# Kernel tuning notes

Hardware: AMD Instinct MI355X
Metric: run time of the kernel (lower is better)

## Reference

```python
import jax, jax.numpy as jnp
import numpy as np

N = 50000
E = 800000
IN_DIM = 128
EMB_DIM = 64
HID = 128
OUT_DIM = 64
VOCAB = 1000
NUM_GRAPHS = 128


def _gat(x, src, dst, W, a_s, a_d, b, n):
    # PyG GATConv, heads=1: h = x @ W (no bias); alpha_e = leaky_relu(a_s.h_src + a_d.h_dst, 0.2)
    h = x @ W                                  # [n, C]
    as_n = h @ a_s                             # [n]
    ad_n = h @ a_d                             # [n]
    logit = jax.nn.leaky_relu(as_n[src] + ad_n[dst], negative_slope=0.2)  # [E']
    # segment softmax over destination node
    m = jax.ops.segment_max(logit, dst, num_segments=n)
    e = jnp.exp(logit - m[dst])
    s = jax.ops.segment_sum(e, dst, num_segments=n)
    coef = e / s[dst]                          # [E']
    out = jax.ops.segment_sum(h[src] * coef[:, None], dst, num_segments=n)
    return out + b


def setup_inputs() -> dict:
    key = jax.random.key(0)
    ks = jax.random.split(key, 20)
    inp = {
        "x": jax.random.normal(ks[0], (N, IN_DIM), dtype=jnp.float32),
        "node_index": jax.random.randint(ks[1], (N,), 0, VOCAB),
        "edge_index": jax.random.randint(ks[2], (2, E), 0, N),
        "batch": jnp.sort(jax.random.randint(ks[3], (N,), 0, NUM_GRAPHS)),
        "emb": jax.random.normal(ks[4], (VOCAB, EMB_DIM), dtype=jnp.float32) * 0.1,
        "W1": jax.random.normal(ks[5], (IN_DIM + EMB_DIM, HID), dtype=jnp.float32) * 0.05,
        "a1s": jax.random.normal(ks[6], (HID,), dtype=jnp.float32) * 0.1,
        "a1d": jax.random.normal(ks[7], (HID,), dtype=jnp.float32) * 0.1,
        "b1": jnp.zeros((HID,), dtype=jnp.float32),
        "W2": jax.random.normal(ks[8], (HID, HID), dtype=jnp.float32) * 0.05,
        "a2s": jax.random.normal(ks[9], (HID,), dtype=jnp.float32) * 0.1,
        "a2d": jax.random.normal(ks[10], (HID,), dtype=jnp.float32) * 0.1,
        "b2": jnp.zeros((HID,), dtype=jnp.float32),
        "W3": jax.random.normal(ks[11], (HID, HID), dtype=jnp.float32) * 0.05,
        "a3s": jax.random.normal(ks[12], (HID,), dtype=jnp.float32) * 0.1,
        "a3d": jax.random.normal(ks[13], (HID,), dtype=jnp.float32) * 0.1,
        "b3": jnp.zeros((HID,), dtype=jnp.float32),
        "fcW": jax.random.normal(ks[14], (HID, OUT_DIM), dtype=jnp.float32) * 0.05,
        "fcb": jnp.zeros((OUT_DIM,), dtype=jnp.float32),
    }
    return inp


def reference(x, node_index, edge_index, batch, emb, W1, a1s, a1d, b1,
              W2, a2s, a2d, b2, W3, a3s, a3d, b3, fcW, fcb):
    n = x.shape[0]
    # embedding lookup + L2 normalize features, then concat
    ev = emb[node_index]                       # [N, EMB_DIM]
    norms = jnp.linalg.norm(x, axis=1, keepdims=True)
    norms = jnp.where(norms == 0, 1e-8, norms)
    h = jnp.concatenate([x / norms, ev], axis=1)  # [N, IN+EMB]
    # add self loops (PyG GATConv default add_self_loops=True)
    loop = jnp.arange(n)
    src = jnp.concatenate([edge_index[0], loop])
    dst = jnp.concatenate([edge_index[1], loop])
    h = jax.nn.gelu(_gat(h, src, dst, W1, a1s, a1d, b1, n))
    h = jax.nn.gelu(_gat(h, src, dst, W2, a2s, a2d, b2, n))
    h = jax.nn.gelu(_gat(h, src, dst, W3, a3s, a3d, b3, n))
    # global_add_pool over graphs
    g = jax.ops.segment_sum(h, batch, num_segments=NUM_GRAPHS)  # [G, HID]
    out = g @ fcW + fcb
    return jax.nn.leaky_relu(out, negative_slope=0.01)
```

## Files before the change

kernel.cpp:

```cpp
#include <hip/hip_runtime.h>

#define N_NODES 50000
#define N_EDGES 800000
#define IN_DIM 128
#define EMB_DIM 64
#define HID 128
#define OUT_DIM 64
#define NUM_GRAPHS 128
#define E_TOT (N_EDGES + N_NODES)
#define K1 (IN_DIM + EMB_DIM)
#define NB 391
#define EPT 16
#define EPB (256 * EPT)

typedef __attribute__((ext_vector_type(8))) short bf16x8;
typedef __attribute__((ext_vector_type(4))) float f32x4;

__device__ __forceinline__ float gelu_f(float x) {
    float x3 = x * x * x;
    return 0.5f * x * (1.0f + tanhf(0.7978845608028654f * (x + 0.044715f * x3)));
}
__device__ __forceinline__ float lrelu02(float x) { return x > 0.f ? x : 0.2f * x; }
__device__ __forceinline__ float rl_f(float v, int j) {
    return __int_as_float(__builtin_amdgcn_readlane(__float_as_int(v), j));
}
__device__ __forceinline__ unsigned short f2bf(float f) {
    unsigned u = __float_as_uint(f);
    unsigned r = (u + 0x7fffu + ((u >> 16) & 1u)) >> 16;
    return (unsigned short)r;
}
__device__ __forceinline__ unsigned pk2bf(float a, float b) {
    return (unsigned)f2bf(a) | ((unsigned)f2bf(b) << 16);
}

__global__ __launch_bounds__(256) void k_prepA(const float* __restrict__ x, const int* __restrict__ nidx,
                                               const float* __restrict__ emb, unsigned* __restrict__ Abu) {
    int lane = threadIdx.x & 63;
    int node = (blockIdx.x * 256 + threadIdx.x) >> 6;
    if (node >= N_NODES) return;
    float2 v = ((const float2*)(x + (size_t)node * IN_DIM))[lane];
    float ss = v.x * v.x + v.y * v.y;
#pragma unroll
    for (int o = 32; o; o >>= 1) ss += __shfl_xor(ss, o);
    float nrm = sqrtf(ss);
    if (nrm == 0.f) nrm = 1e-8f;
    float inv = 1.f / nrm;
    unsigned* row = Abu + (size_t)node * (K1 / 2);
    row[lane] = pk2bf(v.x * inv, v.y * inv);
    int nid = __builtin_amdgcn_readfirstlane(nidx[node]);
    if (lane < 32) {
        float2 e = ((const float2*)(emb + (size_t)nid * EMB_DIM))[lane];
        row[64 + lane] = pk2bf(e.x, e.y);
    }
}

__global__ __launch_bounds__(128) void k_prepW(const float* __restrict__ W, unsigned short* __restrict__ Wt,
                                               int K, int KP) {
    int k = blockIdx.x;
    int c = threadIdx.x;
    Wt[(size_t)c * KP + k] = f2bf(W[(size_t)k * HID + c]);
}

__global__ __launch_bounds__(256) void k_bhist(const int* __restrict__ dst, int* __restrict__ bcnt) {
    __shared__ int h[NB];
    for (int i = threadIdx.x; i < NB; i += 256) h[i] = 0;
    __syncthreads();
    for (int e = blockIdx.x * 256 + threadIdx.x; e < N_EDGES; e += gridDim.x * 256)
        atomicAdd(&h[dst[e] >> 7], 1);
    __syncthreads();
    for (int i = threadIdx.x; i < NB; i += 256)
        if (h[i]) atomicAdd(&bcnt[i], h[i]);
}

__global__ __launch_bounds__(512) void k_bscan(const int* __restrict__ bcnt, int* __restrict__ boff,
                                               int* __restrict__ rowptr) {
    __shared__ int sh[512];
    int t = threadIdx.x;
    int v = (t < NB) ? bcnt[t] : 0;
    sh[t] = v;
    __syncthreads();
    for (int o = 1; o < 512; o <<= 1) {
        int u = (t >= o) ? sh[t - o] : 0;
        __syncthreads();
        sh[t] += u;
        __syncthreads();
    }
    if (t < NB) boff[t] = sh[t] - v;
    if (t == NB - 1) boff[NB] = sh[t];
    if (t == 0) rowptr[N_NODES] = E_TOT;
}

__global__ __launch_bounds__(256) void k_passA(const int* __restrict__ src, const int* __restrict__ dst,
                                               const int* __restrict__ boff, int* __restrict__ bfill,
                                               unsigned* __restrict__ barr) {
    __shared__ int h[NB];
    __shared__ int base[NB];
    for (int i = threadIdx.x; i < NB; i += 256) h[i] = 0;
    __syncthreads();
    int e0 = blockIdx.x * EPB;
    int tag[EPT];
#pragma unroll
    for (int i = 0; i < EPT; i++) {
        int e = e0 + i * 256 + threadIdx.x;
        tag[i] = -1;
        if (e < N_EDGES) {
            int b = dst[e] >> 7;
            int r = atomicAdd(&h[b], 1);
            tag[i] = (b << 12) | r;
        }
    }
    __syncthreads();
    for (int i = threadIdx.x; i < NB; i += 256)
        base[i] = h[i] ? atomicAdd(&bfill[i], h[i]) : 0;
    __syncthreads();
#pragma unroll
    for (int i = 0; i < EPT; i++) {
        if (tag[i] >= 0) {
            int e = e0 + i * 256 + threadIdx.x;
            int b = tag[i] >> 12, r = tag[i] & 0xfff;
            unsigned s = (unsigned)src[e];
            unsigned dl = (unsigned)(dst[e] & 127);
            barr[boff[b] + base[b] + r] = s | (dl << 16);
        }
    }
}

__global__ __launch_bounds__(256) void k_passB(const unsigned* __restrict__ barr, const int* __restrict__ boff,
                                               int* __restrict__ rowptr, int* __restrict__ csr) {
    __shared__ int dcnt[128];
    __shared__ int dsum[128];
    __shared__ int locOff[128];
    int b = blockIdx.x;
    int t = threadIdx.x;
    int n0 = b << 7;
    int cnt = min(128, N_NODES - n0);
    int eb = boff[b], ee = boff[b + 1];
    if (t < 128) dcnt[t] = 0;
    __syncthreads();
    for (int i = eb + t; i < ee; i += 256) atomicAdd(&dcnt[barr[i] >> 16], 1);
    __syncthreads();
    int v = 0;
    if (t < 128) {
        v = (t < cnt) ? dcnt[t] + 1 : 0;
        dsum[t] = v;
    }
    __syncthreads();
    for (int o = 1; o < 128; o <<= 1) {
        int u = (t >= o && t < 128) ? dsum[t - o] : 0;
        __syncthreads();
        if (t < 128) dsum[t] += u;
        __syncthreads();
    }
    int csrBase = eb + n0;
    if (t < 128) {
        locOff[t] = dsum[t] - v;
        dcnt[t] = 0;
    }
    if (t < cnt) {
        int loc = dsum[t] - v;
        rowptr[n0 + t] = csrBase + loc;
        csr[csrBase + loc] = n0 + t;
    }
    __syncthreads();
    for (int i = eb + t; i < ee; i += 256) {
        unsigned vv = barr[i];
        int dl = vv >> 16;
        int s = (int)(vv & 0xffffu);
        int k = atomicAdd(&dcnt[dl], 1);
        csr[csrBase + locOff[dl] + 1 + k] = s;
    }
}

template <int K>
__global__ __launch_bounds__(256) void k_mgemm(const unsigned short* __restrict__ Abf,
                                               const unsigned short* __restrict__ WtP,
                                               const float* __restrict__ a_s, const float* __restrict__ a_d,
                                               unsigned short* __restrict__ Hbf,
                                               float* __restrict__ asn, float* __restrict__ adn) {
    constexpr int KP = K + 8;
    __shared__ __align__(16) unsigned short Wl[128 * KP];
    {
        const uint4* gsrc = (const uint4*)WtP;
        uint4* ldst = (uint4*)Wl;
        const int nchunk = 128 * KP * 2 / 16;
        for (int i = threadIdx.x; i < nchunk; i += 256) ldst[i] = gsrc[i];
    }
    __syncthreads();
    int lane = threadIdx.x & 63;
    int wv = threadIdx.x >> 6;
    int rowbase = blockIdx.x * 64 + wv * 16;
    if (rowbase >= N_NODES) return;
    int l15 = lane & 15, quad = lane >> 4;

    f32x4 acc[8];
#pragma unroll
    for (int t = 0; t < 8; t++) acc[t] = (f32x4){0.f, 0.f, 0.f, 0.f};

    const unsigned short* Abase = Abf + (size_t)(rowbase + l15) * K + quad * 8;
#pragma unroll
    for (int k0 = 0; k0 < K; k0 += 32) {
        bf16x8 af = *(const bf16x8*)(Abase + k0);
#pragma unroll
        for (int t = 0; t < 8; t++) {
            bf16x8 bf = *(const bf16x8*)(&Wl[(t * 16 + l15) * KP + k0 + quad * 8]);
            acc[t] = __builtin_amdgcn_mfma_f32_16x16x32_bf16(af, bf, acc[t], 0, 0, 0);
        }
    }
    float asc[8], adc[8];
#pragma unroll
    for (int t = 0; t < 8; t++) { asc[t] = a_s[t * 16 + l15]; adc[t] = a_d[t * 16 + l15]; }
#pragma unroll
    for (int r = 0; r < 4; r++) {
        int row = rowbase + quad * 4 + r;
        float ps = 0.f, pd = 0.f;
#pragma unroll
        for (int t = 0; t < 8; t++) {
            float v = acc[t][r];
            Hbf[(size_t)row * HID + t * 16 + l15] = f2bf(v);
            ps = fmaf(v, asc[t], ps);
            pd = fmaf(v, adc[t], pd);
        }
#pragma unroll
        for (int o = 1; o < 16; o <<= 1) {
            ps += __shfl_xor(ps, o);
            pd += __shfl_xor(pd, o);
        }
        if (l15 == 0) { asn[row] = ps; adn[row] = pd; }
    }
}

template <bool OUT32>
__global__ __launch_bounds__(256) void k_aggr(const int* __restrict__ rowptr, const int* __restrict__ csr,
                                              const float* __restrict__ asn, const float* __restrict__ adn,
                                              const unsigned short* __restrict__ hbf,
                                              const float* __restrict__ bias, void* __restrict__ outp) {
    __shared__ float sh_e[4][64];
    __shared__ int sh_s[4][64];
    int lane = threadIdx.x & 63;
    int w = threadIdx.x >> 6;
    int node = blockIdx.x * 4 + w;
    if (node >= N_NODES) return;
    int st = rowptr[node], en = rowptr[node + 1];
    int deg = en - st;
    float ad = adn[node];
    const unsigned* hu = (const unsigned*)hbf;
    float2 acc = make_float2(0.f, 0.f);

    if (deg <= 64) {
        int s = 0;
        float l = -1e30f;
        if (lane < deg) {
            s = csr[st + lane];
            l = lrelu02(asn[s] + ad);
        }
        float m = l;
#pragma unroll
        for (int o = 32; o; o >>= 1) m = fmaxf(m, __shfl_xor(m, o));
        float e = (lane < deg) ? __expf(l - m) : 0.f;
        float ssum = e;
#pragma unroll
        for (int o = 32; o; o >>= 1) ssum += __shfl_xor(ssum, o);
        float coef = e / ssum;
        int j = 0;
        for (; j + 4 <= deg; j += 4) {
            int s0 = __builtin_amdgcn_readlane(s, j);
            int s1 = __builtin_amdgcn_readlane(s, j + 1);
            int s2 = __builtin_amdgcn_readlane(s, j + 2);
            int s3 = __builtin_amdgcn_readlane(s, j + 3);
            float c0 = rl_f(coef, j), c1 = rl_f(coef, j + 1);
            float c2 = rl_f(coef, j + 2), c3 = rl_f(coef, j + 3);
            unsigned v0 = hu[(size_t)s0 * 64 + lane];
            unsigned v1 = hu[(size_t)s1 * 64 + lane];
            unsigned v2 = hu[(size_t)s2 * 64 + lane];
            unsigned v3 = hu[(size_t)s3 * 64 + lane];
            acc.x = fmaf(c0, __int_as_float(v0 << 16), acc.x);
            acc.y = fmaf(c0, __int_as_float(v0 & 0xffff0000u), acc.y);
            acc.x = fmaf(c1, __int_as_float(v1 << 16), acc.x);
            acc.y = fmaf(c1, __int_as_float(v1 & 0xffff0000u), acc.y);
            acc.x = fmaf(c2, __int_as_float(v2 << 16), acc.x);
            acc.y = fmaf(c2, __int_as_float(v2 & 0xffff0000u), acc.y);
            acc.x = fmaf(c3, __int_as_float(v3 << 16), acc.x);
            acc.y = fmaf(c3, __int_as_float(v3 & 0xffff0000u), acc.y);
        }
        for (; j < deg; j++) {
            int s0 = __builtin_amdgcn_readlane(s, j);
            float c0 = rl_f(coef, j);
            unsigned v0 = hu[(size_t)s0 * 64 + lane];
            acc.x = fmaf(c0, __int_as_float(v0 << 16), acc.x);
            acc.y = fmaf(c0, __int_as_float(v0 & 0xffff0000u), acc.y);
        }
    } else {
        float m = -1e30f;
        for (int i = st + lane; i < en; i += 64) {
            float l = lrelu02(asn[csr[i]] + ad);
            m = fmaxf(m, l);
        }
#pragma unroll
        for (int o = 32; o; o >>= 1) m = fmaxf(m, __shfl_xor(m, o));
        float ssum = 0.f;
        for (int i = st + lane; i < en; i += 64) {
            float l = lrelu02(asn[csr[i]] + ad);
            ssum += __expf(l - m);
        }
#pragma unroll
        for (int o = 32; o; o >>= 1) ssum += __shfl_xor(ssum, o);
        float inv = 1.f / ssum;
        for (int base = st; base < en; base += 64) {
            int cnt = min(64, en - base);
            if (lane < cnt) {
                int s = csr[base + lane];
                float l = lrelu02(asn[s] + ad);
                sh_e[w][lane] = __expf(l - m) * inv;
                sh_s[w][lane] = s;
            }
            for (int j = 0; j < cnt; j++) {
                float c = sh_e[w][j];
                int s = sh_s[w][j];
                unsigned v0 = hu[(size_t)s * 64 + lane];
                acc.x = fmaf(c, __int_as_float(v0 << 16), acc.x);
                acc.y = fmaf(c, __int_as_float(v0 & 0xffff0000u), acc.y);
            }
        }
    }
    float2 b = ((const float2*)bias)[lane];
    float rx = gelu_f(acc.x + b.x);
    float ry = gelu_f(acc.y + b.y);
    if constexpr (OUT32) {
        ((float2*)outp)[(size_t)node * 64 + lane] = make_float2(rx, ry);
    } else {
        ((unsigned*)outp)[(size_t)node * 64 + lane] = pk2bf(rx, ry);
    }
}

__global__ __launch_bounds__(128) void k_pool(const float* __restrict__ h, const int* __restrict__ batch,
                                              float* __restrict__ g) {
    int c = threadIdx.x;
    int n0 = blockIdx.x * 128;
    if (n0 >= N_NODES) return;
    int n1 = min(n0 + 128, N_NODES);
    int cur = batch[n0];
    float acc = 0.f;
    for (int n = n0; n < n1; n++) {
        int b = batch[n];
        if (b != cur) {
            atomicAdd(&g[cur * HID + c], acc);
            acc = 0.f;
            cur = b;
        }
        acc += h[(size_t)n * HID + c];
    }
    atomicAdd(&g[cur * HID + c], acc);
}

__global__ __launch_bounds__(256) void k_fc(const float* __restrict__ g, const float* __restrict__ fcW,
                                            const float* __restrict__ fcb, float* __restrict__ out) {
    int tid = blockIdx.x * 256 + threadIdx.x;
    if (tid >= NUM_GRAPHS * OUT_DIM) return;
    int gr = tid >> 6;
    int c = tid & 63;
    float acc = fcb[c];
    const float* grow = g + gr * HID;
#pragma unroll 4
    for (int k = 0; k < HID; k++) acc = fmaf(grow[k], fcW[k * OUT_DIM + c], acc);
    out[tid] = acc > 0.f ? acc : 0.01f * acc;
}

extern "C" void kernel_launch(void* const* d_in, const int* in_sizes, int n_in,
                              void* d_out, int out_size, void* d_ws, size_t ws_size,
                              hipStream_t stream) {
    const float* x    = (const float*)d_in[0];
    const int* nidx   = (const int*)d_in[1];
    const int* ei     = (const int*)d_in[2];
    const int* batch  = (const int*)d_in[3];
    const float* emb  = (const float*)d_in[4];
    const float* W1   = (const float*)d_in[5];
    const float* a1s  = (const float*)d_in[6];
    const float* a1d  = (const float*)d_in[7];
    const float* b1   = (const float*)d_in[8];
    const float* W2   = (const float*)d_in[9];
    const float* a2s  = (const float*)d_in[10];
    const float* a2d  = (const float*)d_in[11];
    const float* b2   = (const float*)d_in[12];
    const float* W3   = (const float*)d_in[13];
    const float* a3s  = (const float*)d_in[14];
    const float* a3d  = (const float*)d_in[15];
    const float* b3   = (const float*)d_in[16];
    const float* fcW  = (const float*)d_in[17];
    const float* fcb  = (const float*)d_in[18];
    float* out = (float*)d_out;
    const int* srcA = ei;
    const int* dstA = ei + N_EDGES;

    char* w = (char*)d_ws;
    auto alloc = [&](size_t bytes) -> char* {
        char* p = w;
        w += (bytes + 511) & ~(size_t)511;
        return p;
    };
    char* region0 = alloc((size_t)N_NODES * HID * 4);
    unsigned* Abu = (unsigned*)region0;
    float* h3f    = (float*)region0;
    unsigned short* hLin = (unsigned short*)alloc((size_t)N_NODES * HID * 2);
    unsigned short* hAct = (unsigned short*)alloc((size_t)N_NODES * HID * 2);
    float* asn   = (float*)alloc((size_t)N_NODES * 4);
    float* adn   = (float*)alloc((size_t)N_NODES * 4);
    int* rowptr  = (int*)alloc((size_t)(N_NODES + 1) * 4);
    int* bcnt    = (int*)alloc((size_t)NB * 4);
    int* boff    = (int*)alloc((size_t)(NB + 1) * 4);
    int* bfill   = (int*)alloc((size_t)NB * 4);
    unsigned* barr = (unsigned*)alloc((size_t)N_EDGES * 4);
    int* csr     = (int*)alloc((size_t)E_TOT * 4);
    float* g     = (float*)alloc((size_t)NUM_GRAPHS * HID * 4);
    unsigned short* Wt1 = (unsigned short*)alloc((size_t)HID * (K1 + 8) * 2);
    unsigned short* Wt2 = (unsigned short*)alloc((size_t)HID * (HID + 8) * 2);
    unsigned short* Wt3 = (unsigned short*)alloc((size_t)HID * (HID + 8) * 2);

    hipMemsetAsync(bcnt, 0, (size_t)NB * 4, stream);
    hipMemsetAsync(bfill, 0, (size_t)NB * 4, stream);
    hipMemsetAsync(g, 0, (size_t)NUM_GRAPHS * HID * 4, stream);

    k_prepW<<<K1, 128, 0, stream>>>(W1, Wt1, K1, K1 + 8);
    k_prepW<<<HID, 128, 0, stream>>>(W2, Wt2, HID, HID + 8);
    k_prepW<<<HID, 128, 0, stream>>>(W3, Wt3, HID, HID + 8);
    k_prepA<<<(N_NODES + 3) / 4, 256, 0, stream>>>(x, nidx, emb, Abu);

    k_bhist<<<512, 256, 0, stream>>>(dstA, bcnt);
    k_bscan<<<1, 512, 0, stream>>>(bcnt, boff, rowptr);
    k_passA<<<(N_EDGES + EPB - 1) / EPB, 256, 0, stream>>>(srcA, dstA, boff, bfill, barr);
    k_passB<<<NB, 256, 0, stream>>>(barr, boff, rowptr, csr);

    int gemmBlocks = (N_NODES + 63) / 64;
    int aggrBlocks = (N_NODES + 3) / 4;

    k_mgemm<K1><<<gemmBlocks, 256, 0, stream>>>((const unsigned short*)Abu, Wt1, a1s, a1d, hLin, asn, adn);
    k_aggr<false><<<aggrBlocks, 256, 0, stream>>>(rowptr, csr, asn, adn, hLin, b1, hAct);
    k_mgemm<HID><<<gemmBlocks, 256, 0, stream>>>(hAct, Wt2, a2s, a2d, hLin, asn, adn);
    k_aggr<false><<<aggrBlocks, 256, 0, stream>>>(rowptr, csr, asn, adn, hLin, b2, hAct);
    k_mgemm<HID><<<gemmBlocks, 256, 0, stream>>>(hAct, Wt3, a3s, a3d, hLin, asn, adn);
    k_aggr<true><<<aggrBlocks, 256, 0, stream>>>(rowptr, csr, asn, adn, hLin, b3, h3f);

    k_pool<<<(N_NODES + 127) / 128, 128, 0, stream>>>(h3f, batch, g);
    k_fc<<<(NUM_GRAPHS * OUT_DIM + 255) / 256, 256, 0, stream>>>(g, fcW, fcb, out);
}
```

Baseline: 372.6 us.

## Merge launches, prefetch GEMM A fragments, unroll gather by 8, fuse pool+fc

Three memsets become one zeroing kernel, and the three weight-transpose launches become one kernel. The GEMM now loads all A fragments before the shared-memory barrier, so global loads overlap the weight staging. The aggregation loop gathers eight neighbours at a time to keep more loads in flight. Pooling and the final FC are fused into one block per graph that binary-searches the sorted batch vector, removing atomics and a launch but leaving only 128 blocks for the pooling pass.

```diff
diff --git a/kernel.cpp b/kernel.cpp
--- a/kernel.cpp
+++ b/kernel.cpp
@@ -33,6 +33,27 @@
     return (unsigned)f2bf(a) | ((unsigned)f2bf(b) << 16);
 }
 
+__global__ __launch_bounds__(256) void k_zero(int* __restrict__ bcnt, int* __restrict__ bfill) {
+    int t = blockIdx.x * 256 + threadIdx.x;
+    if (t < NB) { bcnt[t] = 0; bfill[t] = 0; }
+}
+
+__global__ __launch_bounds__(128) void k_prepW3(const float* __restrict__ W1, unsigned short* __restrict__ Wt1,
+                                                const float* __restrict__ W2, unsigned short* __restrict__ Wt2,
+                                                const float* __restrict__ W3, unsigned short* __restrict__ Wt3) {
+    int b = blockIdx.x;
+    int c = threadIdx.x;
+    if (b < K1) {
+        Wt1[(size_t)c * (K1 + 8) + b] = f2bf(W1[(size_t)b * HID + c]);
+    } else if (b < K1 + HID) {
+        int k = b - K1;
+        Wt2[(size_t)c * (HID + 8) + k] = f2bf(W2[(size_t)k * HID + c]);
+    } else {
+        int k = b - K1 - HID;
+        Wt3[(size_t)c * (HID + 8) + k] = f2bf(W3[(size_t)k * HID + c]);
+    }
+}
+
 __global__ __launch_bounds__(256) void k_prepA(const float* __restrict__ x, const int* __restrict__ nidx,
                                                const float* __restrict__ emb, unsigned* __restrict__ Abu) {
     int lane = threadIdx.x & 63;
@@ -52,13 +73,6 @@
         float2 e = ((const float2*)(emb + (size_t)nid * EMB_DIM))[lane];
         row[64 + lane] = pk2bf(e.x, e.y);
     }
-}
-
-__global__ __launch_bounds__(128) void k_prepW(const float* __restrict__ W, unsigned short* __restrict__ Wt,
-                                               int K, int KP) {
-    int k = blockIdx.x;
-    int c = threadIdx.x;
-    Wt[(size_t)c * KP + k] = f2bf(W[(size_t)k * HID + c]);
 }
 
 __global__ __launch_bounds__(256) void k_bhist(const int* __restrict__ dst, int* __restrict__ bcnt) {
@@ -178,6 +192,7 @@
                                                unsigned short* __restrict__ Hbf,
                                                float* __restrict__ asn, float* __restrict__ adn) {
     constexpr int KP = K + 8;
+    constexpr int NK = K / 32;
     __shared__ __align__(16) unsigned short Wl[128 * KP];
     {
         const uint4* gsrc = (const uint4*)WtP;
@@ -185,25 +200,28 @@
         const int nchunk = 128 * KP * 2 / 16;
         for (int i = threadIdx.x; i < nchunk; i += 256) ldst[i] = gsrc[i];
     }
-    __syncthreads();
     int lane = threadIdx.x & 63;
     int wv = threadIdx.x >> 6;
     int rowbase = blockIdx.x * 64 + wv * 16;
-    if (rowbase >= N_NODES) return;
+    if (rowbase >= N_NODES) { __syncthreads(); return; }
     int l15 = lane & 15, quad = lane >> 4;
 
+    const unsigned short* Abase = Abf + (size_t)(rowbase + l15) * K + quad * 8;
+    bf16x8 afr[NK];
+#pragma unroll
+    for (int i = 0; i < NK; i++) afr[i] = *(const bf16x8*)(Abase + i * 32);
+
+    __syncthreads();
+
     f32x4 acc[8];
 #pragma unroll
     for (int t = 0; t < 8; t++) acc[t] = (f32x4){0.f, 0.f, 0.f, 0.f};
-
-    const unsigned short* Abase = Abf + (size_t)(rowbase + l15) * K + quad * 8;
-#pragma unroll
-    for (int k0 = 0; k0 < K; k0 += 32) {
-        bf16x8 af = *(const bf16x8*)(Abase + k0);
+#pragma unroll
+    for (int i = 0; i < NK; i++) {
 #pragma unroll
         for (int t = 0; t < 8; t++) {
-            bf16x8 bf = *(const bf16x8*)(&Wl[(t * 16 + l15) * KP + k0 + quad * 8]);
-            acc[t] = __builtin_amdgcn_mfma_f32_16x16x32_bf16(af, bf, acc[t], 0, 0, 0);
+            bf16x8 bf = *(const bf16x8*)(&Wl[(t * 16 + l15) * KP + i * 32 + quad * 8]);
+            acc[t] = __builtin_amdgcn_mfma_f32_16x16x32_bf16(afr[i], bf, acc[t], 0, 0, 0);
         }
     }
     float asc[8], adc[8];
@@ -262,6 +280,23 @@
         for (int o = 32; o; o >>= 1) ssum += __shfl_xor(ssum, o);
         float coef = e / ssum;
         int j = 0;
+        for (; j + 8 <= deg; j += 8) {
+            int si[8];
+            float ci[8];
+            unsigned vi[8];
+#pragma unroll
+            for (int q = 0; q < 8; q++) {
+                si[q] = __builtin_amdgcn_readlane(s, j + q);
+                ci[q] = rl_f(coef, j + q);
+            }
+#pragma unroll
+            for (int q = 0; q < 8; q++) vi[q] = hu[(size_t)si[q] * 64 + lane];
+#pragma unroll
+            for (int q = 0; q < 8; q++) {
+                acc.x = fmaf(ci[q], __int_as_float(vi[q] << 16), acc.x);
+                acc.y = fmaf(ci[q], __int_as_float(vi[q] & 0xffff0000u), acc.y);
+            }
+        }
         for (; j + 4 <= deg; j += 4) {
             int s0 = __builtin_amdgcn_readlane(s, j);
             int s1 = __builtin_amdgcn_readlane(s, j + 1);
@@ -308,15 +343,15 @@
         for (int base = st; base < en; base += 64) {
             int cnt = min(64, en - base);
             if (lane < cnt) {
-                int s = csr[base + lane];
-                float l = lrelu02(asn[s] + ad);
+                int sx = csr[base + lane];
+                float l = lrelu02(asn[sx] + ad);
                 sh_e[w][lane] = __expf(l - m) * inv;
-                sh_s[w][lane] = s;
+                sh_s[w][lane] = sx;
             }
             for (int j = 0; j < cnt; j++) {
                 float c = sh_e[w][j];
-                int s = sh_s[w][j];
-                unsigned v0 = hu[(size_t)s * 64 + lane];
+                int sx = sh_s[w][j];
+                unsigned v0 = hu[(size_t)sx * 64 + lane];
                 acc.x = fmaf(c, __int_as_float(v0 << 16), acc.x);
                 acc.y = fmaf(c, __int_as_float(v0 & 0xffff0000u), acc.y);
             }
@@ -332,37 +367,36 @@
     }
 }
 
-__global__ __launch_bounds__(128) void k_pool(const float* __restrict__ h, const int* __restrict__ batch,
-                                              float* __restrict__ g) {
-    int c = threadIdx.x;
-    int n0 = blockIdx.x * 128;
-    if (n0 >= N_NODES) return;
-    int n1 = min(n0 + 128, N_NODES);
-    int cur = batch[n0];
+__global__ __launch_bounds__(256) void k_poolfc(const float* __restrict__ h, const int* __restrict__ batch,
+                                                const float* __restrict__ fcW, const float* __restrict__ fcb,
+                                                float* __restrict__ out) {
+    __shared__ float gv[HID];
+    __shared__ float tmp[256];
+    int g = blockIdx.x;
+    int st, en;
+    {
+        int lo = 0, hi = N_NODES;
+        while (lo < hi) { int mid = (lo + hi) >> 1; if (batch[mid] < g) lo = mid + 1; else hi = mid; }
+        st = lo;
+        lo = st; hi = N_NODES;
+        while (lo < hi) { int mid = (lo + hi) >> 1; if (batch[mid] < g + 1) lo = mid + 1; else hi = mid; }
+        en = lo;
+    }
+    int c = threadIdx.x & 127;
+    int half = threadIdx.x >> 7;
     float acc = 0.f;
-    for (int n = n0; n < n1; n++) {
-        int b = batch[n];
-        if (b != cur) {
-            atomicAdd(&g[cur * HID + c], acc);
-            acc = 0.f;
-            cur = b;
-        }
-        acc += h[(size_t)n * HID + c];
-    }
-    atomicAdd(&g[cur * HID + c], acc);
-}
-
-__global__ __launch_bounds__(256) void k_fc(const float* __restrict__ g, const float* __restrict__ fcW,
-                                            const float* __restrict__ fcb, float* __restrict__ out) {
-    int tid = blockIdx.x * 256 + threadIdx.x;
-    if (tid >= NUM_GRAPHS * OUT_DIM) return;
-    int gr = tid >> 6;
-    int c = tid & 63;
-    float acc = fcb[c];
-    const float* grow = g + gr * HID;
 #pragma unroll 4
-    for (int k = 0; k < HID; k++) acc = fmaf(grow[k], fcW[k * OUT_DIM + c], acc);
-    out[tid] = acc > 0.f ? acc : 0.01f * acc;
+    for (int n = st + half; n < en; n += 2) acc += h[(size_t)n * HID + c];
+    tmp[threadIdx.x] = acc;
+    __syncthreads();
+    if (threadIdx.x < HID) gv[threadIdx.x] = tmp[threadIdx.x] + tmp[threadIdx.x + 128];
+    __syncthreads();
+    if (threadIdx.x < OUT_DIM) {
+        float a = fcb[threadIdx.x];
+#pragma unroll 4
+        for (int k = 0; k < HID; k++) a = fmaf(gv[k], fcW[k * OUT_DIM + threadIdx.x], a);
+        out[g * OUT_DIM + threadIdx.x] = a > 0.f ? a : 0.01f * a;
+    }
 }
 
 extern "C" void kernel_launch(void* const* d_in, const int* in_sizes, int n_in,
@@ -410,18 +444,12 @@
     int* bfill   = (int*)alloc((size_t)NB * 4);
     unsigned* barr = (unsigned*)alloc((size_t)N_EDGES * 4);
     int* csr     = (int*)alloc((size_t)E_TOT * 4);
-    float* g     = (float*)alloc((size_t)NUM_GRAPHS * HID * 4);
     unsigned short* Wt1 = (unsigned short*)alloc((size_t)HID * (K1 + 8) * 2);
     unsigned short* Wt2 = (unsigned short*)alloc((size_t)HID * (HID + 8) * 2);
     unsigned short* Wt3 = (unsigned short*)alloc((size_t)HID * (HID + 8) * 2);
 
-    hipMemsetAsync(bcnt, 0, (size_t)NB * 4, stream);
-    hipMemsetAsync(bfill, 0, (size_t)NB * 4, stream);
-    hipMemsetAsync(g, 0, (size_t)NUM_GRAPHS * HID * 4, stream);
-
-    k_prepW<<<K1, 128, 0, stream>>>(W1, Wt1, K1, K1 + 8);
-    k_prepW<<<HID, 128, 0, stream>>>(W2, Wt2, HID, HID + 8);
-    k_prepW<<<HID, 128, 0, stream>>>(W3, Wt3, HID, HID + 8);
+    k_zero<<<(NB + 255) / 256, 256, 0, stream>>>(bcnt, bfill);
+    k_prepW3<<<K1 + 2 * HID, 128, 0, stream>>>(W1, Wt1, W2, Wt2, W3, Wt3);
     k_prepA<<<(N_NODES + 3) / 4, 256, 0, stream>>>(x, nidx, emb, Abu);
 
     k_bhist<<<512, 256, 0, stream>>>(dstA, bcnt);
@@ -439,6 +467,5 @@
     k_mgemm<HID><<<gemmBlocks, 256, 0, stream>>>(hAct, Wt3, a3s, a3d, hLin, asn, adn);
     k_aggr<true><<<aggrBlocks, 256, 0, stream>>>(rowptr, csr, asn, adn, hLin, b3, h3f);
 
-    k_pool<<<(N_NODES + 127) / 128, 128, 0, stream>>>(h3f, batch, g);
-    k_fc<<<(NUM_GRAPHS * OUT_DIM + 255) / 256, 256, 0, stream>>>(g, fcW, fcb, out);
-}
+    k_poolfc<<<NUM_GRAPHS, 256, 0, stream>>>(h3f, batch, fcW, fcb, out);
+}
```

Result: faster. 334.3 us (-10.3%).
